# Kernel optimization log

Hardware: AMD Instinct MI355X
Metric: run time of the kernel (lower is better)

The kernel has to match this reference:

```python
import jax, jax.numpy as jnp
import numpy as np

NUM_EXPERTS = 8
EXPERTS_PER_TOK = 2

def setup_inputs() -> dict:
    key = jax.random.key(0)
    k1, k2, k3, k4, k5 = jax.random.split(key, 5)
    B, T, D, F, E = 4, 1024, 2048, 1024, NUM_EXPERTS
    return {
        "x": jax.random.normal(k1, (B, T, D), dtype=jnp.float32),
        "router_w": jax.random.normal(k2, (D, E), dtype=jnp.float32) * 0.02,
        "gate_proj": jax.random.normal(k3, (E, D, F), dtype=jnp.float32) * 0.02,
        "up_proj": jax.random.normal(k4, (E, D, F), dtype=jnp.float32) * 0.02,
        "down_proj": jax.random.normal(k5, (E, F, D), dtype=jnp.float32) * 0.02,
    }

def reference(x, router_w, gate_proj, up_proj, down_proj):
    E, K = NUM_EXPERTS, EXPERTS_PER_TOK
    # Router: softmax over experts, take top-k, renormalize.
    scores = jnp.einsum('btd,de->bte', x, router_w).astype(jnp.float32)
    routing_weights, routing_idx = jax.lax.top_k(jax.nn.softmax(scores, axis=-1), K)
    routing_weights = (routing_weights / jnp.sum(routing_weights, axis=-1, keepdims=True)).astype(x.dtype)
    # one_hot: [B,T,K,E]. Sum over K gives 0/1 dispatch mask [B,T,E]
    # (top-k indices are distinct). Weighted sum gives combine weights.
    onehot = jax.nn.one_hot(routing_idx, E, dtype=x.dtype)
    dispatch_mask = jnp.sum(onehot, axis=2)                      # [B,T,E]
    combine_weights = jnp.einsum('btke,btk->bte', onehot, routing_weights)
    # Dense masked dispatch (same math as original einsum with size-1 I axis).
    dispatched = x[:, :, None, :] * dispatch_mask[..., None]     # [B,T,E,D]
    # SwiGLU FFN for every expert, batched over E.
    gate = jnp.einsum('bted,edf->btef', dispatched, gate_proj)
    up = jnp.einsum('bted,edf->btef', dispatched, up_proj)
    act = jax.nn.silu(gate) * up                                 # [B,T,E,F]
    expert_out = jnp.einsum('btef,efd->bted', act, down_proj)    # [B,T,E,D]
    # Combine: weights already include the dispatch mask via one-hot.
    return jnp.einsum('bted,bte->btd', expert_out, combine_weights)
```

## Files before the change

### kernel.cpp

```cpp
#include <hip/hip_runtime.h>
#include <stdint.h>

#define BT 4096
#define DMODEL 2048
#define FDIM 1024
#define NEXP 8
#define NA (BT * 2)
#define MAXTILES 72

typedef __attribute__((ext_vector_type(8))) __bf16 bf16x8;
typedef __attribute__((ext_vector_type(4))) float f32x4;

__device__ __forceinline__ unsigned short f2bf(float f) {
  union { float f; unsigned int u; } v; v.f = f;
  unsigned int u = v.u;
  unsigned int r = (u + 0x7fffu + ((u >> 16) & 1u)) >> 16;
  return (unsigned short)r;
}
__device__ __forceinline__ float bf2f(unsigned short h) {
  union { unsigned int u; float f; } v; v.u = ((unsigned int)h) << 16;
  return v.f;
}

__device__ __forceinline__ void g2l16(const void* g, void* l) {
  __builtin_amdgcn_global_load_lds((const __attribute__((address_space(1))) void*)g,
                                   (__attribute__((address_space(3))) void*)l, 16, 0, 0);
}


__global__ void k_router(const float* __restrict__ x, const float* __restrict__ rw,
                         unsigned short* __restrict__ xbf,
                         int* __restrict__ tok_e, float* __restrict__ tok_w) {
  int wid = threadIdx.x >> 6;
  int lane = threadIdx.x & 63;
  int t = blockIdx.x * 4 + wid;
  float acc[8];
#pragma unroll
  for (int e = 0; e < 8; e++) acc[e] = 0.0f;
  const float* xr = x + (size_t)t * DMODEL;
  unsigned short* xbr = xbf + (size_t)t * DMODEL;
  for (int d = lane; d < DMODEL; d += 64) {
    float xv = xr[d];
    xbr[d] = f2bf(xv);
    const float4* r4 = (const float4*)(rw + d * NEXP);
    float4 ra = r4[0], rb = r4[1];
    acc[0] += xv * ra.x; acc[1] += xv * ra.y; acc[2] += xv * ra.z; acc[3] += xv * ra.w;
    acc[4] += xv * rb.x; acc[5] += xv * rb.y; acc[6] += xv * rb.z; acc[7] += xv * rb.w;
  }
#pragma unroll
  for (int e = 0; e < 8; e++) {
    float v = acc[e];
#pragma unroll
    for (int off = 32; off > 0; off >>= 1) v += __shfl_xor(v, off);
    acc[e] = v;
  }
  if (lane == 0) {
    int e0 = 0; float s0 = acc[0];
#pragma unroll
    for (int e = 1; e < 8; e++) if (acc[e] > s0) { s0 = acc[e]; e0 = e; }
    int e1 = (e0 == 0) ? 1 : 0; float s1 = acc[e1];
#pragma unroll
    for (int e = 0; e < 8; e++) if (e != e0 && acc[e] > s1) { s1 = acc[e]; e1 = e; }
    float w0 = 1.0f / (1.0f + __expf(s1 - s0));
    tok_e[t * 2] = e0; tok_e[t * 2 + 1] = e1;
    tok_w[t * 2] = w0; tok_w[t * 2 + 1] = 1.0f - w0;
  }
}

__global__ void k_scanbuild(const int* __restrict__ tok_e, int* __restrict__ offsets,
                            int* __restrict__ tile_e, int* __restrict__ tile_y,
                            int* __restrict__ ntiles, int* __restrict__ cursors) {
  __shared__ int hist[NEXP];
  int tid = threadIdx.x;
  if (tid < NEXP) hist[tid] = 0;
  __syncthreads();
  for (int i = tid; i < NA; i += 256) atomicAdd(&hist[tok_e[i]], 1);
  __syncthreads();
  if (tid == 0) {
    int s = 0;
    for (int e = 0; e < NEXP; e++) { offsets[e] = s; s += hist[e]; }
    offsets[NEXP] = s;
    int idx = 0;
    for (int e = 0; e < NEXP; e++) {
      int nt = (hist[e] + 127) >> 7;
      for (int y = 0; y < nt; y++) { tile_e[idx] = e; tile_y[idx] = y; idx++; }
    }
    *ntiles = idx;
    for (int i = idx; i < MAXTILES; i++) { tile_e[i] = 0; tile_y[i] = 0; }
  }
  if (tid < NEXP) cursors[tid] = 0;
}

__global__ void k_scatter(const int* __restrict__ tok_e, const float* __restrict__ tok_w,
                          const int* __restrict__ offsets, int* __restrict__ cursors,
                          int* __restrict__ assign_token, float* __restrict__ assign_w,
                          int* __restrict__ tok2pos) {
  int i = blockIdx.x * 256 + threadIdx.x;
  if (i >= NA) return;
  int e = tok_e[i];
  int pos = offsets[e] + atomicAdd(&cursors[e], 1);
  assign_token[pos] = i >> 1;
  assign_w[pos] = tok_w[i];
  tok2pos[i] = pos;
}

__global__ void k_transpose_all(const float* __restrict__ gw, const float* __restrict__ uw,
                                const float* __restrict__ dw,
                                unsigned short* __restrict__ wtg, unsigned short* __restrict__ wtu,
                                unsigned short* __restrict__ wtd) {
  __shared__ float tile[64][65];
  int z = blockIdx.y;
  const float* src; unsigned short* dst; int N;
  if (z < 8)       { src = gw + (size_t)z * DMODEL * FDIM;        dst = wtg + (size_t)z * DMODEL * FDIM;        N = FDIM; }
  else if (z < 16) { src = uw + (size_t)(z - 8) * DMODEL * FDIM;  dst = wtu + (size_t)(z - 8) * DMODEL * FDIM;  N = FDIM; }
  else             { src = dw + (size_t)(z - 16) * FDIM * DMODEL; dst = wtd + (size_t)(z - 16) * FDIM * DMODEL; N = DMODEL; }
  int ntx = N >> 6;
  int bx = blockIdx.x;
  int n0 = (bx % ntx) * 64, k0 = (bx / ntx) * 64;
  int rr = threadIdx.x >> 4, cc = threadIdx.x & 15;
#pragma unroll
  for (int i = 0; i < 4; i++) {
    int k = rr + i * 16;
    float4 v = *(const float4*)(src + (size_t)(k0 + k) * N + n0 + cc * 4);
    tile[k][cc * 4 + 0] = v.x; tile[k][cc * 4 + 1] = v.y;
    tile[k][cc * 4 + 2] = v.z; tile[k][cc * 4 + 3] = v.w;
  }
  __syncthreads();
  int K = (z < 16) ? DMODEL : FDIM;
#pragma unroll
  for (int i = 0; i < 4; i++) {
    int n = rr + i * 16;
    ushort4 o = make_ushort4(f2bf(tile[cc * 4 + 0][n]), f2bf(tile[cc * 4 + 1][n]),
                             f2bf(tile[cc * 4 + 2][n]), f2bf(tile[cc * 4 + 3][n]));
    *(ushort4*)(dst + (size_t)(n0 + n) * K + k0 + cc * 4) = o;
  }
}


__global__ __launch_bounds__(512, 4) void k_gemm1(
    const unsigned short* __restrict__ xbf,
    const unsigned short* __restrict__ wtg,
    const unsigned short* __restrict__ wtu,
    const int* __restrict__ offsets,
    const int* __restrict__ tile_e, const int* __restrict__ tile_y,
    const int* __restrict__ ntiles,
    const int* __restrict__ assign_token,
    unsigned short* __restrict__ act) {
  const int ti = blockIdx.y;
  if (ti >= *ntiles) return;
  const int e = tile_e[ti];
  const int row_beg = offsets[e], row_end = offsets[e + 1];
  const int m_base = row_beg + tile_y[ti] * 128;
  const int n_base = blockIdx.x * 128;

  __shared__ unsigned short As[128][64];
  __shared__ unsigned short Bg[128][64];
  __shared__ unsigned short Bu[128][64];

  const int tid = threadIdx.x;
  const int lane = tid & 63, wid = tid >> 6;
  const int wr = wid >> 1, wc = wid & 1;
  const int srow = tid >> 3;
  const int scol_d = (tid & 7) * 8;
  const int scol_s = ((tid & 7) ^ (srow & 7)) * 8;
  const int sw = (lane & 7) * 8;

  const unsigned short* wg_e = wtg + (size_t)e * FDIM * DMODEL;
  const unsigned short* wu_e = wtu + (size_t)e * FDIM * DMODEL;

  size_t arow[2];
#pragma unroll
  for (int r = 0; r < 2; r++) {
    int slot = m_base + r * 64 + srow;
    if (slot >= row_end) slot = row_end - 1;
    arow[r] = (size_t)assign_token[slot] * DMODEL;
  }

  f32x4 accg[2][4], accu[2][4];
#pragma unroll
  for (int m = 0; m < 2; m++)
#pragma unroll
    for (int n = 0; n < 4; n++) {
      accg[m][n] = f32x4{0.f, 0.f, 0.f, 0.f};
      accu[m][n] = f32x4{0.f, 0.f, 0.f, 0.f};
    }

  for (int k0 = 0; k0 < DMODEL; k0 += 64) {
    __syncthreads();
#pragma unroll
    for (int r = 0; r < 2; r++)
      g2l16(xbf + arow[r] + k0 + scol_s, &As[r * 64 + srow][scol_d]);
#pragma unroll
    for (int r = 0; r < 2; r++)
      g2l16(wg_e + (size_t)(n_base + r * 64 + srow) * DMODEL + k0 + scol_s, &Bg[r * 64 + srow][scol_d]);
#pragma unroll
    for (int r = 0; r < 2; r++)
      g2l16(wu_e + (size_t)(n_base + r * 64 + srow) * DMODEL + k0 + scol_s, &Bu[r * 64 + srow][scol_d]);
    __syncthreads();

#pragma unroll
    for (int kk = 0; kk < 2; kk++) {
      const int ko = kk * 32 + (lane >> 4) * 8;
      bf16x8 a[2];
#pragma unroll
      for (int m = 0; m < 2; m++)
        a[m] = *(const bf16x8*)&As[wr * 32 + m * 16 + (lane & 15)][ko ^ sw];
      {
        bf16x8 b[4];
#pragma unroll
        for (int n = 0; n < 4; n++)
          b[n] = *(const bf16x8*)&Bg[wc * 64 + n * 16 + (lane & 15)][ko ^ sw];
#pragma unroll
        for (int m = 0; m < 2; m++)
#pragma unroll
          for (int n = 0; n < 4; n++)
            accg[m][n] = __builtin_amdgcn_mfma_f32_16x16x32_bf16(a[m], b[n], accg[m][n], 0, 0, 0);
      }
      {
        bf16x8 b[4];
#pragma unroll
        for (int n = 0; n < 4; n++)
          b[n] = *(const bf16x8*)&Bu[wc * 64 + n * 16 + (lane & 15)][ko ^ sw];
#pragma unroll
        for (int m = 0; m < 2; m++)
#pragma unroll
          for (int n = 0; n < 4; n++)
            accu[m][n] = __builtin_amdgcn_mfma_f32_16x16x32_bf16(a[m], b[n], accu[m][n], 0, 0, 0);
      }
    }
  }

  const int cr = (lane >> 4) * 4;
  const int ccc = lane & 15;
#pragma unroll
  for (int m = 0; m < 2; m++) {
#pragma unroll
    for (int j = 0; j < 4; j++) {
      int slot = m_base + wr * 32 + m * 16 + cr + j;
      if (slot < row_end) {
        unsigned short* dst = act + (size_t)slot * FDIM + n_base + wc * 64 + ccc;
#pragma unroll
        for (int n = 0; n < 4; n++) {
          float g = accg[m][n][j], u = accu[m][n][j];
          float h = (g / (1.0f + __expf(-g))) * u;
          dst[n * 16] = f2bf(h);
        }
      }
    }
  }
}


__global__ __launch_bounds__(256, 4) void k_gemm2(
    const unsigned short* __restrict__ act,
    const unsigned short* __restrict__ wtd,
    const int* __restrict__ offsets,
    const int* __restrict__ tile_e, const int* __restrict__ tile_y,
    const int* __restrict__ ntiles,
    const float* __restrict__ assign_w,
    unsigned short* __restrict__ out_pa) {
  const int ti = blockIdx.y;
  if (ti >= *ntiles) return;
  const int e = tile_e[ti];
  const int row_beg = offsets[e], row_end = offsets[e + 1];
  const int m_base = row_beg + tile_y[ti] * 128;
  const int n_base = blockIdx.x * 128;

  __shared__ unsigned short As[128][64];
  __shared__ unsigned short Bs[128][64];

  const int tid = threadIdx.x;
  const int lane = tid & 63, wid = tid >> 6;
  const int wr = wid >> 1, wc = wid & 1;
  const int srow = wid * 8 + (lane >> 3);
  const int scol_d = (lane & 7) * 8;
  const int scol_s = ((lane & 7) ^ (lane >> 3)) * 8;
  const int sw = (lane & 7) * 8;

  const unsigned short* wd_e = wtd + (size_t)e * DMODEL * FDIM;

  size_t arow[4];
#pragma unroll
  for (int i = 0; i < 4; i++) {
    int slot = m_base + i * 32 + srow;
    if (slot >= row_end) slot = row_end - 1;
    arow[i] = (size_t)slot * FDIM;
  }

  f32x4 acc[4][4];
#pragma unroll
  for (int m = 0; m < 4; m++)
#pragma unroll
    for (int n = 0; n < 4; n++) acc[m][n] = f32x4{0.f, 0.f, 0.f, 0.f};

  for (int k0 = 0; k0 < FDIM; k0 += 64) {
    __syncthreads();
#pragma unroll
    for (int i = 0; i < 4; i++)
      g2l16(act + arow[i] + k0 + scol_s, &As[i * 32 + srow][scol_d]);
#pragma unroll
    for (int i = 0; i < 4; i++)
      g2l16(wd_e + (size_t)(n_base + i * 32 + srow) * FDIM + k0 + scol_s, &Bs[i * 32 + srow][scol_d]);
    __syncthreads();

#pragma unroll
    for (int kk = 0; kk < 2; kk++) {
      const int ko = kk * 32 + (lane >> 4) * 8;
      bf16x8 a[4], b[4];
#pragma unroll
      for (int m = 0; m < 4; m++)
        a[m] = *(const bf16x8*)&As[wr * 64 + m * 16 + (lane & 15)][ko ^ sw];
#pragma unroll
      for (int n = 0; n < 4; n++)
        b[n] = *(const bf16x8*)&Bs[wc * 64 + n * 16 + (lane & 15)][ko ^ sw];
#pragma unroll
      for (int m = 0; m < 4; m++)
#pragma unroll
        for (int n = 0; n < 4; n++)
          acc[m][n] = __builtin_amdgcn_mfma_f32_16x16x32_bf16(a[m], b[n], acc[m][n], 0, 0, 0);
    }
  }

  const int cr = (lane >> 4) * 4;
  const int ccc = lane & 15;
#pragma unroll
  for (int m = 0; m < 4; m++) {
#pragma unroll
    for (int j = 0; j < 4; j++) {
      int slot = m_base + wr * 64 + m * 16 + cr + j;
      if (slot < row_end) {
        float w = assign_w[slot];
        unsigned short* dst = out_pa + (size_t)slot * DMODEL + n_base + wc * 64 + ccc;
#pragma unroll
        for (int n = 0; n < 4; n++)
          dst[n * 16] = f2bf(acc[m][n][j] * w);
      }
    }
  }
}

__global__ void k_combine(const unsigned short* __restrict__ out_pa,
                          const int* __restrict__ tok2pos,
                          float* __restrict__ out) {
  int t = blockIdx.x;
  int p0 = tok2pos[t * 2], p1 = tok2pos[t * 2 + 1];
  int c = threadIdx.x;
  const ushort4* a = (const ushort4*)(out_pa + (size_t)p0 * DMODEL + c * 8);
  const ushort4* b = (const ushort4*)(out_pa + (size_t)p1 * DMODEL + c * 8);
  ushort4 a0 = a[0], a1 = a[1], b0 = b[0], b1 = b[1];
  float* o = out + (size_t)t * DMODEL + c * 8;
  o[0] = bf2f(a0.x) + bf2f(b0.x);
  o[1] = bf2f(a0.y) + bf2f(b0.y);
  o[2] = bf2f(a0.z) + bf2f(b0.z);
  o[3] = bf2f(a0.w) + bf2f(b0.w);
  o[4] = bf2f(a1.x) + bf2f(b1.x);
  o[5] = bf2f(a1.y) + bf2f(b1.y);
  o[6] = bf2f(a1.z) + bf2f(b1.z);
  o[7] = bf2f(a1.w) + bf2f(b1.w);
}


extern "C" void kernel_launch(void* const* d_in, const int* in_sizes, int n_in,
                              void* d_out, int out_size, void* d_ws, size_t ws_size,
                              hipStream_t stream) {
  const float* x  = (const float*)d_in[0];
  const float* rw = (const float*)d_in[1];
  const float* gw = (const float*)d_in[2];
  const float* uw = (const float*)d_in[3];
  const float* dw = (const float*)d_in[4];
  float* out = (float*)d_out;

  char* ws = (char*)d_ws;
  size_t off = 0;
  auto alloc = [&](size_t bytes) {
    size_t o = off;
    off += (bytes + 255) & ~(size_t)255;
    return o;
  };
  unsigned short* xbf    = (unsigned short*)(ws + alloc((size_t)BT * DMODEL * 2));
  unsigned short* wtg    = (unsigned short*)(ws + alloc((size_t)NEXP * FDIM * DMODEL * 2));
  unsigned short* wtu    = (unsigned short*)(ws + alloc((size_t)NEXP * FDIM * DMODEL * 2));
  unsigned short* wtd    = (unsigned short*)(ws + alloc((size_t)NEXP * DMODEL * FDIM * 2));
  unsigned short* act    = (unsigned short*)(ws + alloc((size_t)NA * FDIM * 2));
  unsigned short* out_pa = (unsigned short*)(ws + alloc((size_t)NA * DMODEL * 2));
  int*   offsets = (int*)(ws + alloc((NEXP + 1) * 4));
  int*   cursors = (int*)(ws + alloc(NEXP * 4));
  int*   tok_e   = (int*)(ws + alloc(NA * 4));
  float* tok_w   = (float*)(ws + alloc(NA * 4));
  int*   assign_token = (int*)(ws + alloc(NA * 4));
  float* assign_w     = (float*)(ws + alloc(NA * 4));
  int*   tok2pos      = (int*)(ws + alloc(NA * 4));
  int*   tile_e       = (int*)(ws + alloc(MAXTILES * 4));
  int*   tile_y       = (int*)(ws + alloc(MAXTILES * 4));
  int*   ntiles       = (int*)(ws + alloc(4));
  if (off > ws_size) return;

  k_router<<<BT / 4, 256, 0, stream>>>(x, rw, xbf, tok_e, tok_w);
  k_scanbuild<<<1, 256, 0, stream>>>(tok_e, offsets, tile_e, tile_y, ntiles, cursors);
  k_scatter<<<NA / 256, 256, 0, stream>>>(tok_e, tok_w, offsets, cursors,
                                          assign_token, assign_w, tok2pos);
  k_transpose_all<<<dim3(512, 24), 256, 0, stream>>>(gw, uw, dw, wtg, wtu, wtd);
  k_gemm1<<<dim3(FDIM / 128, MAXTILES), 512, 0, stream>>>(xbf, wtg, wtu, offsets,
                                                          tile_e, tile_y, ntiles,
                                                          assign_token, act);
  k_gemm2<<<dim3(DMODEL / 128, MAXTILES), 256, 0, stream>>>(act, wtd, offsets,
                                                            tile_e, tile_y, ntiles,
                                                            assign_w, out_pa);
  k_combine<<<BT, 256, 0, stream>>>(out_pa, tok2pos, out);
}
```

Measured before the change: 300.7 us.

## Enlarge gemm1 per-warp tile, remap grids for XCD locality, vectorize router loads

gemm1 drops from 512 to 256 threads per block, so each warp computes a 64x64 tile of both gate and up outputs with 4x4 MFMA accumulators, which raises operand reuse from LDS. Both GEMM grids are flattened to 1D and block IDs are remapped in strides of 8, likely to keep blocks that share tiles together across MI355X's XCDs for L2 reuse. Launch bounds for both GEMMs drop to 2 blocks per SM. The router now loads x as float4 and writes bf16 as ushort4. Doubling the accumulators raises register pressure and may lower occupancy.

```diff
diff --git a/kernel.cpp b/kernel.cpp
--- a/kernel.cpp
+++ b/kernel.cpp
@@ -7,6 +7,10 @@
 #define NEXP 8
 #define NA (BT * 2)
 #define MAXTILES 72
+#define NB1 (FDIM / 128)
+#define NB2 (DMODEL / 128)
+#define GRID1 (MAXTILES * NB1)
+#define GRID2 (MAXTILES * NB2)
 
 typedef __attribute__((ext_vector_type(8))) __bf16 bf16x8;
 typedef __attribute__((ext_vector_type(4))) float f32x4;
@@ -39,13 +43,20 @@
   for (int e = 0; e < 8; e++) acc[e] = 0.0f;
   const float* xr = x + (size_t)t * DMODEL;
   unsigned short* xbr = xbf + (size_t)t * DMODEL;
-  for (int d = lane; d < DMODEL; d += 64) {
-    float xv = xr[d];
-    xbr[d] = f2bf(xv);
-    const float4* r4 = (const float4*)(rw + d * NEXP);
-    float4 ra = r4[0], rb = r4[1];
-    acc[0] += xv * ra.x; acc[1] += xv * ra.y; acc[2] += xv * ra.z; acc[3] += xv * ra.w;
-    acc[4] += xv * rb.x; acc[5] += xv * rb.y; acc[6] += xv * rb.z; acc[7] += xv * rb.w;
+#pragma unroll
+  for (int d0 = lane * 4; d0 < DMODEL; d0 += 256) {
+    float4 xv = *(const float4*)(xr + d0);
+    ushort4 o = make_ushort4(f2bf(xv.x), f2bf(xv.y), f2bf(xv.z), f2bf(xv.w));
+    *(ushort4*)(xbr + d0) = o;
+    const float* xs = &xv.x;
+#pragma unroll
+    for (int j = 0; j < 4; j++) {
+      const float4* r4 = (const float4*)(rw + (size_t)(d0 + j) * NEXP);
+      float4 ra = r4[0], rb = r4[1];
+      float xj = xs[j];
+      acc[0] += xj * ra.x; acc[1] += xj * ra.y; acc[2] += xj * ra.z; acc[3] += xj * ra.w;
+      acc[4] += xj * rb.x; acc[5] += xj * rb.y; acc[6] += xj * rb.z; acc[7] += xj * rb.w;
+    }
   }
 #pragma unroll
   for (int e = 0; e < 8; e++) {
@@ -137,7 +148,7 @@
 }
 
 
-__global__ __launch_bounds__(512, 4) void k_gemm1(
+__global__ __launch_bounds__(256, 2) void k_gemm1(
     const unsigned short* __restrict__ xbf,
     const unsigned short* __restrict__ wtg,
     const unsigned short* __restrict__ wtu,
@@ -146,12 +157,15 @@
     const int* __restrict__ ntiles,
     const int* __restrict__ assign_token,
     unsigned short* __restrict__ act) {
-  const int ti = blockIdx.y;
+  const int flat = blockIdx.x;
+  const int wgid = (flat & 7) * (GRID1 / 8) + (flat >> 3);
+  const int ti = wgid % MAXTILES;
+  const int nb = wgid / MAXTILES;
   if (ti >= *ntiles) return;
   const int e = tile_e[ti];
   const int row_beg = offsets[e], row_end = offsets[e + 1];
   const int m_base = row_beg + tile_y[ti] * 128;
-  const int n_base = blockIdx.x * 128;
+  const int n_base = nb * 128;
 
   __shared__ unsigned short As[128][64];
   __shared__ unsigned short Bg[128][64];
@@ -160,25 +174,25 @@
   const int tid = threadIdx.x;
   const int lane = tid & 63, wid = tid >> 6;
   const int wr = wid >> 1, wc = wid & 1;
-  const int srow = tid >> 3;
-  const int scol_d = (tid & 7) * 8;
-  const int scol_s = ((tid & 7) ^ (srow & 7)) * 8;
+  const int srow = wid * 8 + (lane >> 3);
+  const int scol_d = (lane & 7) * 8;
+  const int scol_s = ((lane & 7) ^ (lane >> 3)) * 8;
   const int sw = (lane & 7) * 8;
 
   const unsigned short* wg_e = wtg + (size_t)e * FDIM * DMODEL;
   const unsigned short* wu_e = wtu + (size_t)e * FDIM * DMODEL;
 
-  size_t arow[2];
-#pragma unroll
-  for (int r = 0; r < 2; r++) {
-    int slot = m_base + r * 64 + srow;
+  size_t arow[4];
+#pragma unroll
+  for (int i = 0; i < 4; i++) {
+    int slot = m_base + i * 32 + srow;
     if (slot >= row_end) slot = row_end - 1;
-    arow[r] = (size_t)assign_token[slot] * DMODEL;
-  }
-
-  f32x4 accg[2][4], accu[2][4];
-#pragma unroll
-  for (int m = 0; m < 2; m++)
+    arow[i] = (size_t)assign_token[slot] * DMODEL;
+  }
+
+  f32x4 accg[4][4], accu[4][4];
+#pragma unroll
+  for (int m = 0; m < 4; m++)
 #pragma unroll
     for (int n = 0; n < 4; n++) {
       accg[m][n] = f32x4{0.f, 0.f, 0.f, 0.f};
@@ -188,55 +202,45 @@
   for (int k0 = 0; k0 < DMODEL; k0 += 64) {
     __syncthreads();
 #pragma unroll
-    for (int r = 0; r < 2; r++)
-      g2l16(xbf + arow[r] + k0 + scol_s, &As[r * 64 + srow][scol_d]);
-#pragma unroll
-    for (int r = 0; r < 2; r++)
-      g2l16(wg_e + (size_t)(n_base + r * 64 + srow) * DMODEL + k0 + scol_s, &Bg[r * 64 + srow][scol_d]);
-#pragma unroll
-    for (int r = 0; r < 2; r++)
-      g2l16(wu_e + (size_t)(n_base + r * 64 + srow) * DMODEL + k0 + scol_s, &Bu[r * 64 + srow][scol_d]);
+    for (int i = 0; i < 4; i++)
+      g2l16(xbf + arow[i] + k0 + scol_s, &As[i * 32 + srow][scol_d]);
+#pragma unroll
+    for (int i = 0; i < 4; i++)
+      g2l16(wg_e + (size_t)(n_base + i * 32 + srow) * DMODEL + k0 + scol_s, &Bg[i * 32 + srow][scol_d]);
+#pragma unroll
+    for (int i = 0; i < 4; i++)
+      g2l16(wu_e + (size_t)(n_base + i * 32 + srow) * DMODEL + k0 + scol_s, &Bu[i * 32 + srow][scol_d]);
     __syncthreads();
 
 #pragma unroll
     for (int kk = 0; kk < 2; kk++) {
       const int ko = kk * 32 + (lane >> 4) * 8;
-      bf16x8 a[2];
-#pragma unroll
-      for (int m = 0; m < 2; m++)
-        a[m] = *(const bf16x8*)&As[wr * 32 + m * 16 + (lane & 15)][ko ^ sw];
-      {
-        bf16x8 b[4];
-#pragma unroll
-        for (int n = 0; n < 4; n++)
-          b[n] = *(const bf16x8*)&Bg[wc * 64 + n * 16 + (lane & 15)][ko ^ sw];
-#pragma unroll
-        for (int m = 0; m < 2; m++)
-#pragma unroll
-          for (int n = 0; n < 4; n++)
-            accg[m][n] = __builtin_amdgcn_mfma_f32_16x16x32_bf16(a[m], b[n], accg[m][n], 0, 0, 0);
+      bf16x8 a[4], bg[4], bu[4];
+#pragma unroll
+      for (int m = 0; m < 4; m++)
+        a[m] = *(const bf16x8*)&As[wr * 64 + m * 16 + (lane & 15)][ko ^ sw];
+#pragma unroll
+      for (int n = 0; n < 4; n++) {
+        bg[n] = *(const bf16x8*)&Bg[wc * 64 + n * 16 + (lane & 15)][ko ^ sw];
+        bu[n] = *(const bf16x8*)&Bu[wc * 64 + n * 16 + (lane & 15)][ko ^ sw];
       }
-      {
-        bf16x8 b[4];
-#pragma unroll
-        for (int n = 0; n < 4; n++)
-          b[n] = *(const bf16x8*)&Bu[wc * 64 + n * 16 + (lane & 15)][ko ^ sw];
-#pragma unroll
-        for (int m = 0; m < 2; m++)
-#pragma unroll
-          for (int n = 0; n < 4; n++)
-            accu[m][n] = __builtin_amdgcn_mfma_f32_16x16x32_bf16(a[m], b[n], accu[m][n], 0, 0, 0);
-      }
+#pragma unroll
+      for (int m = 0; m < 4; m++)
+#pragma unroll
+        for (int n = 0; n < 4; n++) {
+          accg[m][n] = __builtin_amdgcn_mfma_f32_16x16x32_bf16(a[m], bg[n], accg[m][n], 0, 0, 0);
+          accu[m][n] = __builtin_amdgcn_mfma_f32_16x16x32_bf16(a[m], bu[n], accu[m][n], 0, 0, 0);
+        }
     }
   }
 
   const int cr = (lane >> 4) * 4;
   const int ccc = lane & 15;
 #pragma unroll
-  for (int m = 0; m < 2; m++) {
+  for (int m = 0; m < 4; m++) {
 #pragma unroll
     for (int j = 0; j < 4; j++) {
-      int slot = m_base + wr * 32 + m * 16 + cr + j;
+      int slot = m_base + wr * 64 + m * 16 + cr + j;
       if (slot < row_end) {
         unsigned short* dst = act + (size_t)slot * FDIM + n_base + wc * 64 + ccc;
 #pragma unroll
@@ -251,7 +255,7 @@
 }
 
 
-__global__ __launch_bounds__(256, 4) void k_gemm2(
+__global__ __launch_bounds__(256, 2) void k_gemm2(
     const unsigned short* __restrict__ act,
     const unsigned short* __restrict__ wtd,
     const int* __restrict__ offsets,
@@ -259,12 +263,15 @@
     const int* __restrict__ ntiles,
     const float* __restrict__ assign_w,
     unsigned short* __restrict__ out_pa) {
-  const int ti = blockIdx.y;
+  const int flat = blockIdx.x;
+  const int wgid = (flat & 7) * (GRID2 / 8) + (flat >> 3);
+  const int ti = wgid % MAXTILES;
+  const int nb = wgid / MAXTILES;
   if (ti >= *ntiles) return;
   const int e = tile_e[ti];
   const int row_beg = offsets[e], row_end = offsets[e + 1];
   const int m_base = row_beg + tile_y[ti] * 128;
-  const int n_base = blockIdx.x * 128;
+  const int n_base = nb * 128;
 
   __shared__ unsigned short As[128][64];
   __shared__ unsigned short Bs[128][64];
@@ -400,11 +407,9 @@
   k_scatter<<<NA / 256, 256, 0, stream>>>(tok_e, tok_w, offsets, cursors,
                                           assign_token, assign_w, tok2pos);
   k_transpose_all<<<dim3(512, 24), 256, 0, stream>>>(gw, uw, dw, wtg, wtu, wtd);
-  k_gemm1<<<dim3(FDIM / 128, MAXTILES), 512, 0, stream>>>(xbf, wtg, wtu, offsets,
-                                                          tile_e, tile_y, ntiles,
-                                                          assign_token, act);
-  k_gemm2<<<dim3(DMODEL / 128, MAXTILES), 256, 0, stream>>>(act, wtd, offsets,
-                                                            tile_e, tile_y, ntiles,
-                                                            assign_w, out_pa);
+  k_gemm1<<<GRID1, 256, 0, stream>>>(xbf, wtg, wtu, offsets,
+                                     tile_e, tile_y, ntiles, assign_token, act);
+  k_gemm2<<<GRID2, 256, 0, stream>>>(act, wtd, offsets,
+                                     tile_e, tile_y, ntiles, assign_w, out_pa);
   k_combine<<<BT, 256, 0, stream>>>(out_pa, tok2pos, out);
 }
```

New measurement: 320.5 us. 1.07x slower.
